# Performance work log

Measured on AMD Instinct MI355X. Metric: run time of the kernel, lower is better.

## Reference

```python
import jax, jax.numpy as jnp
import numpy as np

B, S, D_MODEL = 1, 2048, 4096
N_HEADS, N_KV_HEADS = 32, 8
HEAD_DIM = D_MODEL // N_HEADS  # 128
N_REP = N_HEADS // N_KV_HEADS  # 4
ROPE_THETA = 500000.0
NEG_INF = -1e9


def setup_inputs() -> dict:
    key = jax.random.key(0)
    ks = jax.random.split(key, 6)
    std = 0.02 * (2 * 32) ** (-0.5)
    x = jax.random.normal(ks[0], (B, S, D_MODEL), dtype=jnp.float32)
    wq = jax.random.normal(ks[1], (N_HEADS * HEAD_DIM, D_MODEL), dtype=jnp.float32) * std
    wk = jax.random.normal(ks[2], (N_KV_HEADS * HEAD_DIM, D_MODEL), dtype=jnp.float32) * std
    wv = jax.random.normal(ks[3], (N_KV_HEADS * HEAD_DIM, D_MODEL), dtype=jnp.float32) * std
    wo = jax.random.normal(ks[4], (D_MODEL, N_HEADS * HEAD_DIM), dtype=jnp.float32) * std
    cache_k = jnp.zeros((B, S, N_KV_HEADS, HEAD_DIM), dtype=jnp.float32)
    cache_v = jnp.zeros((B, S, N_KV_HEADS, HEAD_DIM), dtype=jnp.float32)
    # RoPE tables: freqs_cis[t, j] = exp(i * t * theta^(-2j/head_dim)), j < head_dim/2
    inv_freq = 1.0 / (ROPE_THETA ** (jnp.arange(0, HEAD_DIM, 2, dtype=jnp.float32) / HEAD_DIM))
    t = jnp.arange(S, dtype=jnp.float32)
    ang = jnp.outer(t, inv_freq)  # [S, HEAD_DIM/2]
    freqs_cos = jnp.cos(ang)
    freqs_sin = jnp.sin(ang)
    # causal additive mask [1, 1, S, S]
    mask = jnp.triu(jnp.full((S, S), NEG_INF, dtype=jnp.float32), k=1)[None, None]
    return {"x": x, "wq": wq, "wk": wk, "wv": wv, "wo": wo,
            "cache_k": cache_k, "cache_v": cache_v,
            "freqs_cos": freqs_cos, "freqs_sin": freqs_sin,
            "mask": mask, "start_pos": 0}


def _apply_rope(x, cos, sin):
    # x: [B, S, H, D]; cos/sin: [S, D/2]; pairs (x[2j], x[2j+1]) form complex numbers
    b, s, h, d = x.shape
    x2 = x.astype(jnp.float32).reshape(b, s, h, d // 2, 2)
    xr, xi = x2[..., 0], x2[..., 1]
    c = cos[None, :, None, :]
    sn = sin[None, :, None, :]
    out_r = xr * c - xi * sn
    out_i = xr * sn + xi * c
    return jnp.stack([out_r, out_i], axis=-1).reshape(b, s, h, d)


def reference(x, wq, wk, wv, wo, cache_k, cache_v, freqs_cos, freqs_sin, mask, start_pos):
    bsz, seq_len, _ = x.shape
    xq = (x @ wq.T).reshape(bsz, seq_len, N_HEADS, HEAD_DIM)
    xk = (x @ wk.T).reshape(bsz, seq_len, N_KV_HEADS, HEAD_DIM)
    xv = (x @ wv.T).reshape(bsz, seq_len, N_KV_HEADS, HEAD_DIM)
    xq = _apply_rope(xq, freqs_cos, freqs_sin)
    xk = _apply_rope(xk, freqs_cos, freqs_sin)
    # KV-cache update then read back the valid prefix
    cache_k = jax.lax.dynamic_update_slice(cache_k, xk, (0, start_pos, 0, 0))
    cache_v = jax.lax.dynamic_update_slice(cache_v, xv, (0, start_pos, 0, 0))
    keys = cache_k[:, : start_pos + seq_len]      # [B, K, KVH, D]
    values = cache_v[:, : start_pos + seq_len]
    # repeat_kv: expand kv heads to match query heads
    keys = jnp.repeat(keys, N_REP, axis=2)        # [B, K, H, D]
    values = jnp.repeat(values, N_REP, axis=2)
    q = xq.transpose(0, 2, 1, 3)                  # [B, H, S, D]
    k = keys.transpose(0, 2, 1, 3)                # [B, H, K, D]
    v = values.transpose(0, 2, 1, 3)
    scores = jnp.einsum('bhqd,bhkd->bhqk', q, k) / jnp.float32(np.sqrt(HEAD_DIM))
    scores = scores + mask
    probs = jax.nn.softmax(scores.astype(jnp.float32), axis=-1).astype(q.dtype)
    out = jnp.einsum('bhqk,bhkd->bhqd', probs, v)           # [B, H, S, D]
    out = out.transpose(0, 2, 1, 3).reshape(bsz, seq_len, -1)
    return out @ wo.T
```

## Files before the change

### kernel.cpp

```cpp
#include <hip/hip_runtime.h>
#include <cstdint>
#include <cstddef>

typedef __attribute__((ext_vector_type(8))) short  short8;
typedef __attribute__((ext_vector_type(4))) float  floatx4;
typedef __attribute__((ext_vector_type(4))) unsigned short ushort4v;

__device__ __forceinline__ unsigned short f2b(float f) {
  unsigned u = __builtin_bit_cast(unsigned, f);
  u = u + 0x7fffu + ((u >> 16) & 1u);
  return (unsigned short)(u >> 16);
}

__device__ __forceinline__ void gld_lds16(const void* g, void* l) {
  __builtin_amdgcn_global_load_lds(
      (const __attribute__((address_space(1))) unsigned int*)g,
      (__attribute__((address_space(3))) unsigned int*)l,
      16, 0, 0);
}

__device__ __forceinline__ short8 ds_read_b128v(const unsigned short* p) {
  short8 r;
  asm volatile("ds_read_b128 %0, %1"
               : "=v"(r)
               : "v"((const __attribute__((address_space(3))) unsigned short*)p));
  return r;
}

#define LGKM0_FENCE()                                        \
  do {                                                       \
    asm volatile("s_waitcnt lgkmcnt(0)" ::: "memory");       \
    __builtin_amdgcn_sched_barrier(0);                       \
  } while (0)

__global__ void __launch_bounds__(256) f2b_kernel(const float* __restrict__ in,
                                                  unsigned short* __restrict__ out,
                                                  int n4) {
  int i = blockIdx.x * 256 + threadIdx.x;
  if (i >= n4) return;
  floatx4 v = ((const floatx4*)in)[i];
  ushort4v o;
  o[0] = f2b(v[0]); o[1] = f2b(v[1]); o[2] = f2b(v[2]); o[3] = f2b(v[3]);
  ((ushort4v*)out)[i] = o;
}

template <int MODE, int BN>
__global__ void __launch_bounds__(512, 2)
gemm256(const unsigned short* __restrict__ A,
        const unsigned short* __restrict__ B,
        float* __restrict__ Cf,
        unsigned short* __restrict__ Cb,
        int K, int N,
        const float* __restrict__ fc,
        const float* __restrict__ fs) {
  constexpr int BM = 256, BK = 64;
  constexpr int NF  = BN / 64;
  constexpr int WNC = BN / 4;
  constexpr int NB  = BN / 64;

  __shared__ __align__(16) unsigned short As[2][BM * BK];
  __shared__ __align__(16) unsigned short Bs[2][BN * BK];

  const int tid  = threadIdx.x;
  const int wave = tid >> 6, lane = tid & 63;
  const int quad = lane >> 4, l15 = lane & 15;
  const int wr = wave >> 2, wc = wave & 3;

  int flat = blockIdx.y * 8 + blockIdx.x;
  const int cpx = (int)(gridDim.x * gridDim.y) >> 3;
  flat = (flat & 7) * cpx + (flat >> 3);
  const int m0 = (flat & 7) * BM;
  const int n0 = (flat >> 3) * BN;

  const int srow = lane >> 3;
  const int soct = (lane & 7) ^ srow;
  const unsigned short* pa[4];
  const unsigned short* pb[NB];
#pragma unroll
  for (int i = 0; i < 4; ++i)
    pa[i] = A + (size_t)(m0 + wave * 32 + i * 8 + srow) * K + soct * 8;
#pragma unroll
  for (int i = 0; i < NB; ++i)
    pb[i] = B + (size_t)(n0 + wave * (BN / 8) + i * 8 + srow) * K + soct * 8;

  const int xr = l15 & 7;
  int aoff[2], boff[2];
#pragma unroll
  for (int ks = 0; ks < 2; ++ks) {
    const int sl = ((ks * 4 + quad) ^ xr) * 8;
    aoff[ks] = (wr * 128 + l15) * 64 + sl;
    boff[ks] = (wc * WNC + l15) * 64 + sl;
  }

  floatx4 acc[8][NF] = {};
  const int NT = K >> 6;

#pragma unroll
  for (int i = 0; i < 4; ++i)
    gld_lds16(pa[i], &As[0][(wave * 32 + i * 8) * 64]);
#pragma unroll
  for (int i = 0; i < NB; ++i)
    gld_lds16(pb[i], &Bs[0][(wave * (BN / 8) + i * 8) * 64]);
  asm volatile("s_waitcnt vmcnt(0)" ::: "memory");
  __builtin_amdgcn_s_barrier();
  __builtin_amdgcn_sched_barrier(0);

  int t = 0, kt = 0;

#define TILE_STEP(BUF)                                                         \
  do {                                                                         \
          \
    short8 bfr[NF][2], afr[2][2];                                              \
    _Pragma("unroll") for (int n = 0; n < NF; ++n)                             \
      _Pragma("unroll") for (int ks = 0; ks < 2; ++ks)                         \
        bfr[n][ks] = ds_read_b128v(&Bs[BUF][boff[ks] + n * 1024]);             \
    _Pragma("unroll") for (int mm = 0; mm < 2; ++mm)                           \
      _Pragma("unroll") for (int ks = 0; ks < 2; ++ks)                         \
        afr[mm][ks] = ds_read_b128v(&As[BUF][aoff[ks] + mm * 1024]);           \
    if (t + 1 < NT) {                                                          \
      const int kn = kt + 64;                                                  \
      _Pragma("unroll") for (int i = 0; i < 4; ++i)                            \
        gld_lds16(pa[i] + kn, &As[1 - (BUF)][(wave * 32 + i * 8) * 64]);       \
      _Pragma("unroll") for (int i = 0; i < NB; ++i)                           \
        gld_lds16(pb[i] + kn, &Bs[1 - (BUF)][(wave * (BN / 8) + i * 8) * 64]); \
    }                                                                          \
    __builtin_amdgcn_s_barrier();                                              \
    LGKM0_FENCE();                                                             \
    __builtin_amdgcn_s_setprio(1);                                             \
    _Pragma("unroll") for (int mm = 0; mm < 2; ++mm)                           \
      _Pragma("unroll") for (int n = 0; n < NF; ++n)                           \
        _Pragma("unroll") for (int ks = 0; ks < 2; ++ks)                       \
          acc[mm][n] = __builtin_amdgcn_mfma_f32_16x16x32_bf16(                \
              afr[mm][ks], bfr[n][ks], acc[mm][n], 0, 0, 0);                   \
    __builtin_amdgcn_s_setprio(0);                                             \
    __builtin_amdgcn_s_barrier();                                              \
                               \
    _Pragma("unroll") for (int p = 1; p < 4; ++p) {                            \
      short8 a2[2][2];                                                         \
      _Pragma("unroll") for (int mm = 0; mm < 2; ++mm)                         \
        _Pragma("unroll") for (int ks = 0; ks < 2; ++ks)                       \
          a2[mm][ks] =                                                         \
              ds_read_b128v(&As[BUF][aoff[ks] + (p * 2 + mm) * 1024]);         \
      __builtin_amdgcn_s_barrier();                                            \
      LGKM0_FENCE();                                                           \
      __builtin_amdgcn_s_setprio(1);                                           \
      _Pragma("unroll") for (int mm = 0; mm < 2; ++mm)                         \
        _Pragma("unroll") for (int n = 0; n < NF; ++n)                         \
          _Pragma("unroll") for (int ks = 0; ks < 2; ++ks)                     \
            acc[p * 2 + mm][n] = __builtin_amdgcn_mfma_f32_16x16x32_bf16(      \
                a2[mm][ks], bfr[n][ks], acc[p * 2 + mm][n], 0, 0, 0);          \
      __builtin_amdgcn_s_setprio(0);                                           \
      if (p == 3) asm volatile("s_waitcnt vmcnt(0)" ::: "memory");             \
      __builtin_amdgcn_s_barrier();                                            \
    }                                                                          \
    __builtin_amdgcn_sched_barrier(0);                                         \
    kt += 64;                                                                  \
    ++t;                                                                       \
  } while (0)

  while (t < NT) {
    TILE_STEP(0);
    TILE_STEP(1);
  }
#undef TILE_STEP

#pragma unroll
  for (int mi = 0; mi < 8; ++mi) {
#pragma unroll
    for (int n = 0; n < NF; ++n) {
      const int colb = n0 + wc * WNC + n * 16;
      const int col  = colb + l15;
      const bool rope = (MODE == 2) && (colb < 5120);
      const int pp = (col & 127) >> 1;
      const float sgn = (l15 & 1) ? 1.f : -1.f;
#pragma unroll
      for (int r = 0; r < 4; ++r) {
        const int row = m0 + wr * 128 + mi * 16 + quad * 4 + r;
        float v = acc[mi][n][r];
        if (rope) {
          const float partner = __shfl_xor(v, 1);
          const float c  = fc[row * 64 + pp];
          const float sn = fs[row * 64 + pp];
          v = v * c + partner * sn * sgn;
        }
        if (MODE == 1) Cf[(size_t)row * N + col] = v;
        else           Cb[(size_t)row * N + col] = f2b(v);
      }
    }
  }
}

__global__ void __launch_bounds__(256) transpose_bf16(const unsigned short* __restrict__ in,
                                                      unsigned short* __restrict__ out,
                                                      int R, int C, int in_stride) {
  __shared__ __align__(16) unsigned short tile[64][72];
  const int br = blockIdx.y * 64;
  const int bc = blockIdx.x * 64;
  const int tid = threadIdx.x;
  const int lr = tid >> 3;
  const int lc = (tid & 7) * 8;
#pragma unroll
  for (int it = 0; it < 2; ++it) {
    const int r = it * 32 + lr;
    *(short8*)&tile[r][lc] = *(const short8*)(in + (size_t)(br + r) * in_stride + bc + lc);
  }
  __syncthreads();
#pragma unroll
  for (int it = 0; it < 2; ++it) {
    const int c = it * 32 + lr;
    short8 v;
#pragma unroll
    for (int j = 0; j < 8; ++j) v[j] = (short)tile[lc + j][c];
    *(short8*)(out + (size_t)(bc + c) * R + br + lc) = v;
  }
}

#define SL2E 0.1275500406721347f

__global__ void __launch_bounds__(256) flash_attn(const unsigned short* __restrict__ Q,
                                                  const unsigned short* __restrict__ Kp,
                                                  const unsigned short* __restrict__ Vt,
                                                  unsigned short* __restrict__ O) {
  constexpr int QS = 6144;
  const int bx  = blockIdx.x;
  const int h   = blockIdx.y;
  const int kvh = h >> 2;
  const int tid = threadIdx.x;
  const int wave = tid >> 6, lane = tid & 63;
  const int quad = lane >> 4, l15 = lane & 15;

  __shared__ __align__(16) unsigned short Ks[2][8192];
  __shared__ __align__(16) unsigned short Vs[2][8192];
  __shared__ __align__(16) unsigned short Ps[4][16 * 76];
  unsigned short* Pw = Ps[wave];

  const int i0 = wave * 4;
  const unsigned short* kbase = Kp + kvh * 128;
  const unsigned short* vbase[4];
  int vslot_sc[4];
#pragma unroll
  for (int ii = 0; ii < 4; ++ii) {
    const int i = i0 + ii;
    const int slot = i * 64 + lane;
    const int sc = slot >> 7, d = slot & 127;
    vbase[ii] = Vt + (size_t)(kvh * 128 + d) * 2048;
    vslot_sc[ii] = sc * 8;
  }

  for (int seg = 0; seg < 2; ++seg) {
    const int qt  = seg ? (31 - bx) : bx;
    const int q0  = qt * 64;
    const int qra = q0 + wave * 16;
    const int n   = qt + 1;

    short8 aq[4];
#pragma unroll
    for (int ks = 0; ks < 4; ++ks)
      aq[ks] = *(const short8*)(Q + (size_t)(qra + l15) * QS + h * 128 + ks * 32 + quad * 8);

    floatx4 oacc[8] = {};
    float mrow[4], lrow[4];
#pragma unroll
    for (int r = 0; r < 4; ++r) { mrow[r] = -1e30f; lrow[r] = 0.f; }

    {
      const int cc = 0;
#pragma unroll
      for (int ii = 0; ii < 4; ++ii) {
        const int i = i0 + ii;
        gld_lds16(kbase + (size_t)(cc + lane) * QS + i * 8, &Ks[0][i * 512]);
        gld_lds16(vbase[ii] + cc + vslot_sc[ii], &Vs[0][i * 512]);
      }
    }

    for (int j = 0; j < n; ++j) {
      __syncthreads();
      if (j + 1 < n) {
        const int cc = (j + 1) * 64;
        const int nb = (j + 1) & 1;
#pragma unroll
        for (int ii = 0; ii < 4; ++ii) {
          const int i = i0 + ii;
          gld_lds16(kbase + (size_t)(cc + lane) * QS + i * 8, &Ks[nb][i * 512]);
          gld_lds16(vbase[ii] + cc + vslot_sc[ii], &Vs[nb][i * 512]);
        }
      }
      const unsigned short* kb = Ks[j & 1];
      const unsigned short* vb = Vs[j & 1];
      const int c0 = j * 64;

      floatx4 sacc[4] = {};
#pragma unroll
      for (int ks = 0; ks < 4; ++ks) {
#pragma unroll
        for (int tn = 0; tn < 4; ++tn) {
          short8 bk = *(const short8*)&kb[((ks * 4 + quad) * 64 + tn * 16 + l15) * 8];
          sacc[tn] = __builtin_amdgcn_mfma_f32_16x16x32_bf16(aq[ks], bk, sacc[tn], 0, 0, 0);
        }
      }

      const bool needmask = (c0 + 63 > qra);
#pragma unroll
      for (int r = 0; r < 4; ++r) {
        const int rowg = qra + quad * 4 + r;
        float t0 = sacc[0][r] * SL2E, t1 = sacc[1][r] * SL2E;
        float t2 = sacc[2][r] * SL2E, t3 = sacc[3][r] * SL2E;
        if (needmask) {
          t0 = (c0 +  0 + l15 <= rowg) ? t0 : -1e30f;
          t1 = (c0 + 16 + l15 <= rowg) ? t1 : -1e30f;
          t2 = (c0 + 32 + l15 <= rowg) ? t2 : -1e30f;
          t3 = (c0 + 48 + l15 <= rowg) ? t3 : -1e30f;
        }
        float mx = fmaxf(fmaxf(t0, t1), fmaxf(t2, t3));
#pragma unroll
        for (int off = 1; off < 16; off <<= 1)
          mx = fmaxf(mx, __shfl_xor(mx, off, 16));
        const float mold = mrow[r];
        const float mn   = fmaxf(mold, mx);
        const float alpha = exp2f(mold - mn);
        float p0 = exp2f(t0 - mn), p1 = exp2f(t1 - mn);
        float p2 = exp2f(t2 - mn), p3 = exp2f(t3 - mn);
        sacc[0][r] = p0; sacc[1][r] = p1; sacc[2][r] = p2; sacc[3][r] = p3;
        float lsum = (p0 + p1) + (p2 + p3);
#pragma unroll
        for (int off = 1; off < 16; off <<= 1)
          lsum += __shfl_xor(lsum, off, 16);
        mrow[r] = mn;
        lrow[r] = lrow[r] * alpha + lsum;
#pragma unroll
        for (int tn = 0; tn < 8; ++tn) oacc[tn][r] *= alpha;
      }

#pragma unroll
      for (int tn = 0; tn < 4; ++tn)
#pragma unroll
        for (int r = 0; r < 4; ++r)
          Pw[(quad * 4 + r) * 76 + tn * 16 + l15] = f2b(sacc[tn][r]);

      short8 ap[2];
#pragma unroll
      for (int k2 = 0; k2 < 2; ++k2)
        ap[k2] = *(const short8*)&Pw[l15 * 76 + k2 * 32 + quad * 8];
#pragma unroll
      for (int k2 = 0; k2 < 2; ++k2) {
#pragma unroll
        for (int tn = 0; tn < 8; ++tn) {
          short8 bv = *(const short8*)&vb[((k2 * 4 + quad) * 128 + tn * 16 + l15) * 8];
          oacc[tn] = __builtin_amdgcn_mfma_f32_16x16x32_bf16(ap[k2], bv, oacc[tn], 0, 0, 0);
        }
      }
    }

#pragma unroll
    for (int r = 0; r < 4; ++r) {
      const float inv = 1.f / lrow[r];
      const int rowg = qra + quad * 4 + r;
#pragma unroll
      for (int tn = 0; tn < 8; ++tn)
        O[(size_t)rowg * 4096 + h * 128 + tn * 16 + l15] = f2b(oacc[tn][r] * inv);
    }
    __syncthreads();
  }
}

extern "C" void kernel_launch(void* const* d_in, const int* in_sizes, int n_in,
                              void* d_out, int out_size, void* d_ws, size_t ws_size,
                              hipStream_t stream) {
  const float* x  = (const float*)d_in[0];
  const float* wq = (const float*)d_in[1];
  const float* wk = (const float*)d_in[2];
  const float* wv = (const float*)d_in[3];
  const float* wo = (const float*)d_in[4];
  const float* fc = (const float*)d_in[7];
  const float* fs = (const float*)d_in[8];
  float* out = (float*)d_out;

  char* ws = (char*)d_ws;
  unsigned short* xb    = (unsigned short*)(ws + 0);
  unsigned short* wqkvb = (unsigned short*)(ws + 16777216);
  unsigned short* wob   = (unsigned short*)(ws + 67108864);
  unsigned short* qkv   = (unsigned short*)(ws + 100663296);
  unsigned short* vt    = (unsigned short*)(ws + 125829120);
  unsigned short* ob    = (unsigned short*)(ws + 130023424);
  unsigned short* wkb = wqkvb + (size_t)4096 * 4096;
  unsigned short* wvb = wkb + (size_t)1024 * 4096;

  f2b_kernel<<<8192,  256, 0, stream>>>(x,  xb,    2097152);
  f2b_kernel<<<16384, 256, 0, stream>>>(wq, wqkvb, 4194304);
  f2b_kernel<<<4096,  256, 0, stream>>>(wk, wkb,   1048576);
  f2b_kernel<<<4096,  256, 0, stream>>>(wv, wvb,   1048576);
  f2b_kernel<<<16384, 256, 0, stream>>>(wo, wob,   4194304);

  gemm256<2, 192><<<dim3(8, 32), 512, 0, stream>>>(xb, wqkvb, nullptr, qkv,
                                                   4096, 6144, fc, fs);

  transpose_bf16<<<dim3(16, 32), 256, 0, stream>>>(qkv + 5120, vt, 2048, 1024, 6144);

  flash_attn<<<dim3(16, 32), 256, 0, stream>>>(qkv, qkv + 4096, vt, ob);

  gemm256<1, 128><<<dim3(8, 32), 512, 0, stream>>>(ob, wob, out, nullptr,
                                                   4096, 4096, nullptr, nullptr);
}
```

Before: 584.7 us.

## Swizzle flash-attention K/V LDS layout and software-pipeline LDS reads with MFMAs

```diff
diff --git a/kernel.cpp b/kernel.cpp
--- a/kernel.cpp
+++ b/kernel.cpp
@@ -26,12 +26,19 @@
                : "v"((const __attribute__((address_space(3))) unsigned short*)p));
   return r;
 }
-
-#define LGKM0_FENCE()                                        \
+__device__ __forceinline__ void ds_write_b16v(unsigned short* p, unsigned short v) {
+  asm volatile("ds_write_b16 %0, %1"
+               :: "v"((__attribute__((address_space(3))) unsigned short*)p),
+                  "v"((unsigned)v)
+               : "memory");
+}
+
+#define LGKM_FENCE(N)                                        \
   do {                                                       \
-    asm volatile("s_waitcnt lgkmcnt(0)" ::: "memory");       \
+    asm volatile("s_waitcnt lgkmcnt(" #N ")" ::: "memory");  \
     __builtin_amdgcn_sched_barrier(0);                       \
   } while (0)
+#define LGKM0_FENCE() LGKM_FENCE(0)
 
 __global__ void __launch_bounds__(256) f2b_kernel(const float* __restrict__ in,
                                                   unsigned short* __restrict__ out,
@@ -109,7 +116,6 @@
 
 #define TILE_STEP(BUF)                                                         \
   do {                                                                         \
-          \
     short8 bfr[NF][2], afr[2][2];                                              \
     _Pragma("unroll") for (int n = 0; n < NF; ++n)                             \
       _Pragma("unroll") for (int ks = 0; ks < 2; ++ks)                         \
@@ -134,7 +140,6 @@
               afr[mm][ks], bfr[n][ks], acc[mm][n], 0, 0, 0);                   \
     __builtin_amdgcn_s_setprio(0);                                             \
     __builtin_amdgcn_s_barrier();                                              \
-                               \
     _Pragma("unroll") for (int p = 1; p < 4; ++p) {                            \
       short8 a2[2][2];                                                         \
       _Pragma("unroll") for (int mm = 0; mm < 2; ++mm)                         \
@@ -228,29 +233,30 @@
   const int tid = threadIdx.x;
   const int wave = tid >> 6, lane = tid & 63;
   const int quad = lane >> 4, l15 = lane & 15;
+  const int xr8 = l15 & 7;
 
   __shared__ __align__(16) unsigned short Ks[2][8192];
   __shared__ __align__(16) unsigned short Vs[2][8192];
-  __shared__ __align__(16) unsigned short Ps[4][16 * 76];
+  __shared__ __align__(16) unsigned short Ps[4][16 * 88];
   unsigned short* Pw = Ps[wave];
 
-  const int i0 = wave * 4;
-  const unsigned short* kbase = Kp + kvh * 128;
-  const unsigned short* vbase[4];
-  int vslot_sc[4];
+  const unsigned short* kp4[4];
+  const unsigned short* vp4[4];
 #pragma unroll
   for (int ii = 0; ii < 4; ++ii) {
-    const int i = i0 + ii;
-    const int slot = i * 64 + lane;
-    const int sc = slot >> 7, d = slot & 127;
-    vbase[ii] = Vt + (size_t)(kvh * 128 + d) * 2048;
-    vslot_sc[ii] = sc * 8;
+    const int k0   = wave * 16 + ii * 4;
+    const int krow = k0 + (lane >> 4);
+    const int goct = (lane & 15) ^ (krow & 7);
+    kp4[ii] = Kp + kvh * 128 + (size_t)krow * QS + goct * 8;
+    const int d0   = wave * 32 + ii * 8;
+    const int drow = d0 + (lane >> 3);
+    const int voct = (lane & 7) ^ ((lane >> 3) & 7);
+    vp4[ii] = Vt + (size_t)(kvh * 128 + drow) * 2048 + voct * 8;
   }
 
   for (int seg = 0; seg < 2; ++seg) {
     const int qt  = seg ? (31 - bx) : bx;
-    const int q0  = qt * 64;
-    const int qra = q0 + wave * 16;
+    const int qra = qt * 64 + wave * 16;
     const int n   = qt + 1;
 
     short8 aq[4];
@@ -263,40 +269,59 @@
 #pragma unroll
     for (int r = 0; r < 4; ++r) { mrow[r] = -1e30f; lrow[r] = 0.f; }
 
-    {
-      const int cc = 0;
-#pragma unroll
-      for (int ii = 0; ii < 4; ++ii) {
-        const int i = i0 + ii;
-        gld_lds16(kbase + (size_t)(cc + lane) * QS + i * 8, &Ks[0][i * 512]);
-        gld_lds16(vbase[ii] + cc + vslot_sc[ii], &Vs[0][i * 512]);
-      }
+#pragma unroll
+    for (int ii = 0; ii < 4; ++ii) {
+      gld_lds16(kp4[ii], &Ks[0][wave * 2048 + ii * 512]);
+      gld_lds16(vp4[ii], &Vs[0][wave * 2048 + ii * 512]);
     }
 
     for (int j = 0; j < n; ++j) {
-      __syncthreads();
-      if (j + 1 < n) {
-        const int cc = (j + 1) * 64;
-        const int nb = (j + 1) & 1;
-#pragma unroll
-        for (int ii = 0; ii < 4; ++ii) {
-          const int i = i0 + ii;
-          gld_lds16(kbase + (size_t)(cc + lane) * QS + i * 8, &Ks[nb][i * 512]);
-          gld_lds16(vbase[ii] + cc + vslot_sc[ii], &Vs[nb][i * 512]);
-        }
-      }
+      asm volatile("s_waitcnt vmcnt(0)" ::: "memory");
+      __builtin_amdgcn_s_barrier();
+      __builtin_amdgcn_sched_barrier(0);
       const unsigned short* kb = Ks[j & 1];
       const unsigned short* vb = Vs[j & 1];
       const int c0 = j * 64;
 
       floatx4 sacc[4] = {};
-#pragma unroll
-      for (int ks = 0; ks < 4; ++ks) {
-#pragma unroll
-        for (int tn = 0; tn < 4; ++tn) {
-          short8 bk = *(const short8*)&kb[((ks * 4 + quad) * 64 + tn * 16 + l15) * 8];
-          sacc[tn] = __builtin_amdgcn_mfma_f32_16x16x32_bf16(aq[ks], bk, sacc[tn], 0, 0, 0);
-        }
+      {
+        short8 bkA[4], bkB[4];
+#pragma unroll
+        for (int tn = 0; tn < 4; ++tn)
+          bkA[tn] = ds_read_b128v(&kb[(tn * 16 + l15) * 128 + ((quad ^ xr8) * 8)]);
+#pragma unroll
+        for (int tn = 0; tn < 4; ++tn)
+          bkB[tn] = ds_read_b128v(&kb[(tn * 16 + l15) * 128 + (((4 + quad) ^ xr8) * 8)]);
+        LGKM_FENCE(4);
+        __builtin_amdgcn_s_setprio(1);
+#pragma unroll
+        for (int tn = 0; tn < 4; ++tn)
+          sacc[tn] = __builtin_amdgcn_mfma_f32_16x16x32_bf16(aq[0], bkA[tn], sacc[tn], 0, 0, 0);
+        __builtin_amdgcn_s_setprio(0);
+#pragma unroll
+        for (int tn = 0; tn < 4; ++tn)
+          bkA[tn] = ds_read_b128v(&kb[(tn * 16 + l15) * 128 + (((8 + quad) ^ xr8) * 8)]);
+        LGKM_FENCE(4);
+        __builtin_amdgcn_s_setprio(1);
+#pragma unroll
+        for (int tn = 0; tn < 4; ++tn)
+          sacc[tn] = __builtin_amdgcn_mfma_f32_16x16x32_bf16(aq[1], bkB[tn], sacc[tn], 0, 0, 0);
+        __builtin_amdgcn_s_setprio(0);
+#pragma unroll
+        for (int tn = 0; tn < 4; ++tn)
+          bkB[tn] = ds_read_b128v(&kb[(tn * 16 + l15) * 128 + (((12 + quad) ^ xr8) * 8)]);
+        LGKM_FENCE(4);
+        __builtin_amdgcn_s_setprio(1);
+#pragma unroll
+        for (int tn = 0; tn < 4; ++tn)
+          sacc[tn] = __builtin_amdgcn_mfma_f32_16x16x32_bf16(aq[2], bkA[tn], sacc[tn], 0, 0, 0);
+        __builtin_amdgcn_s_setprio(0);
+        LGKM_FENCE(0);
+        __builtin_amdgcn_s_setprio(1);
+#pragma unroll
+        for (int tn = 0; tn < 4; ++tn)
+          sacc[tn] = __builtin_amdgcn_mfma_f32_16x16x32_bf16(aq[3], bkB[tn], sacc[tn], 0, 0, 0);
+        __builtin_amdgcn_s_setprio(0);
       }
 
       const bool needmask = (c0 + 63 > qra);
@@ -331,24 +356,42 @@
         for (int tn = 0; tn < 8; ++tn) oacc[tn][r] *= alpha;
       }
 
-#pragma unroll
-      for (int tn = 0; tn < 4; ++tn)
-#pragma unroll
-        for (int r = 0; r < 4; ++r)
-          Pw[(quad * 4 + r) * 76 + tn * 16 + l15] = f2b(sacc[tn][r]);
-
-      short8 ap[2];
-#pragma unroll
-      for (int k2 = 0; k2 < 2; ++k2)
-        ap[k2] = *(const short8*)&Pw[l15 * 76 + k2 * 32 + quad * 8];
-#pragma unroll
-      for (int k2 = 0; k2 < 2; ++k2) {
-#pragma unroll
-        for (int tn = 0; tn < 8; ++tn) {
-          short8 bv = *(const short8*)&vb[((k2 * 4 + quad) * 128 + tn * 16 + l15) * 8];
-          oacc[tn] = __builtin_amdgcn_mfma_f32_16x16x32_bf16(ap[k2], bv, oacc[tn], 0, 0, 0);
+      if (j + 1 < n) {
+        const int cc = (j + 1) * 64;
+        const int nb = (j + 1) & 1;
+#pragma unroll
+        for (int ii = 0; ii < 4; ++ii) {
+          gld_lds16(kp4[ii] + (size_t)cc * QS, &Ks[nb][wave * 2048 + ii * 512]);
+          gld_lds16(vp4[ii] + cc, &Vs[nb][wave * 2048 + ii * 512]);
         }
       }
+
+#pragma unroll
+      for (int tn = 0; tn < 4; ++tn)
+#pragma unroll
+        for (int r = 0; r < 4; ++r)
+          ds_write_b16v(&Pw[(quad * 4 + r) * 88 + tn * 16 + l15], f2b(sacc[tn][r]));
+      short8 ap0 = ds_read_b128v(&Pw[l15 * 88 + quad * 8]);
+      short8 ap1 = ds_read_b128v(&Pw[l15 * 88 + 32 + quad * 8]);
+      short8 bv0[8], bv1[8];
+#pragma unroll
+      for (int tn = 0; tn < 8; ++tn)
+        bv0[tn] = ds_read_b128v(&vb[(tn * 16 + l15) * 64 + ((quad ^ xr8) * 8)]);
+#pragma unroll
+      for (int tn = 0; tn < 8; ++tn)
+        bv1[tn] = ds_read_b128v(&vb[(tn * 16 + l15) * 64 + (((4 + quad) ^ xr8) * 8)]);
+      LGKM_FENCE(8);
+      __builtin_amdgcn_s_setprio(1);
+#pragma unroll
+      for (int tn = 0; tn < 8; ++tn)
+        oacc[tn] = __builtin_amdgcn_mfma_f32_16x16x32_bf16(ap0, bv0[tn], oacc[tn], 0, 0, 0);
+      __builtin_amdgcn_s_setprio(0);
+      LGKM_FENCE(0);
+      __builtin_amdgcn_s_setprio(1);
+#pragma unroll
+      for (int tn = 0; tn < 8; ++tn)
+        oacc[tn] = __builtin_amdgcn_mfma_f32_16x16x32_bf16(ap1, bv1[tn], oacc[tn], 0, 0, 0);
+      __builtin_amdgcn_s_setprio(0);
     }
 
 #pragma unroll
```

Result: faster. 549.3 us (-6.1%).
